# Kernel optimization log

Measured on AMD Instinct MI355X. Metric: run time of the kernel, lower is better.

The kernel has to match this reference:

```python
import jax, jax.numpy as jnp
import numpy as np

HT_H, HT_W = 512, 512          # Hough accumulator grid
SPHERE_SIZE = 32768            # Gaussian-sphere bins
NUM_VOTES = 1_500_000          # rows in vote_mapping
BATCH, CHANNEL = 2, 64         # channel % 4 == 0 required by the module


def setup_inputs() -> dict:
    key = jax.random.key(0)
    k1, k2, k3, k4 = jax.random.split(key, 4)
    x = jax.random.normal(k1, (BATCH, CHANNEL, HT_H, HT_W), dtype=jnp.float32)
    ht_idx = jax.random.randint(k2, (NUM_VOTES,), 0, HT_H * HT_W, dtype=jnp.int32)
    sphere_idx = jax.random.randint(k3, (NUM_VOTES,), 0, SPHERE_SIZE, dtype=jnp.int32)
    weight = jax.random.uniform(k4, (NUM_VOTES,), dtype=jnp.float32)
    return {"x": x, "ht_idx": ht_idx, "sphere_idx": sphere_idx, "weight": weight}


def reference(x, ht_idx, sphere_idx, weight):
    b, c, h, w = x.shape
    # SPHERE_CUDA.forward: split channels into 4 groups, flatten HT grid
    xf = x.reshape(b * 4, c // 4, h * w)              # [B4, C4, HW]
    # HT2SPHERE: gather each vote's HT cell, scale by vote weight,
    # scatter-add into its sphere bin.
    votes = xf[:, :, ht_idx] * weight                  # [B4, C4, V]
    out = jax.ops.segment_sum(
        jnp.moveaxis(votes, -1, 0), sphere_idx, num_segments=SPHERE_SIZE
    )                                                  # [S, B4, C4]
    out = jnp.moveaxis(out, 0, -1)                     # [B4, C4, S]
    return out.reshape(b, c, SPHERE_SIZE)              # [B, C, S]
```

## Files before the change

kernel.cpp:

```cpp
#include <hip/hip_runtime.h>
#include <stdint.h>


#define S_BINS   32768
#define NBUCKET  1024
#define BINS     32
#define CAP      2048
#define CHUNK    8192
#define MAXRB    192
#define HT_BITS  18

__device__ __forceinline__ unsigned bf16_rne(float f) {
    unsigned u = __float_as_uint(f);
    return (u + 0x7FFFu + ((u >> 16) & 1u)) >> 16;
}

__global__ __launch_bounds__(512) void fused_tr_kernel(
    const float* __restrict__ x, uint32_t* __restrict__ xTb, int HW,
    const int* __restrict__ ht, const int* __restrict__ sp,
    const float* __restrict__ w,
    uint2* __restrict__ records, int* __restrict__ blkcur,
    int V, int nrb) {
    __shared__ __align__(16) char smem[69696];
    const int t = threadIdx.x;
    if ((int)blockIdx.x < nrb) {
        uint2* rec  = (uint2*)smem;
        int*   hcur = (int*)(smem + 65536);
        int*   wsum = (int*)(smem + 69632);
        const int blk = blockIdx.x;
        const int lane = t & 63, wv = t >> 6;
        const int base = blk * CHUNK, end = min(V, base + CHUNK), n = end - base;
        hcur[2 * t] = 0; hcur[2 * t + 1] = 0;
        __syncthreads();
        for (int v = base + t; v < end; v += 512) atomicAdd(&hcur[sp[v] >> 5], 1);
        __syncthreads();
        const int l0 = hcur[2 * t], l1 = hcur[2 * t + 1];
        const int tot = l0 + l1;
        int sc = tot;
#pragma unroll
        for (int off = 1; off < 64; off <<= 1) {
            const int up = __shfl_up(sc, off);
            if (lane >= off) sc += up;
        }
        if (lane == 63) wsum[wv] = sc;
        __syncthreads();
        if (wv == 0 && lane < 8) {
            const int v0 = wsum[lane];
            int s = v0;
#pragma unroll
            for (int off = 1; off < 8; off <<= 1) {
                const int up = __shfl_up(s, off);
                if (lane >= off) s += up;
            }
            wsum[lane] = s - v0;
        }
        __syncthreads();
        const int run = wsum[wv] + (sc - tot);
        hcur[2 * t]     = run;
        hcur[2 * t + 1] = run + l0;
        __syncthreads();
        for (int v = base + t; v < end; v += 512) {
            const int s = sp[v];
            const int b = s >> 5, sl = s & 31;
            const int pos = atomicAdd(&hcur[b], 1);
            rec[pos] = make_uint2((unsigned)ht[v] | ((unsigned)sl << HT_BITS),
                                  __float_as_uint(w[v]));
        }
        __syncthreads();
        for (int i = t; i < n; i += 512)
            records[(size_t)blk * CHUNK + i] = rec[i];
        blkcur[(size_t)blk * NBUCKET + 2 * t]     = hcur[2 * t];
        blkcur[(size_t)blk * NBUCKET + 2 * t + 1] = hcur[2 * t + 1];
    } else {
        float* tile = (float*)smem;
        const int ht0 = ((int)blockIdx.x - nrb) * 64;
        for (int e = t; e < 128 * 16; e += 512) {
            const int ch = e >> 4, hq = e & 15;
            const float4 v = *(const float4*)(x + (size_t)ch * HW + ht0 + 4 * hq);
            const int a = 4 * hq;
            tile[(a + 0) * 129 + ch] = v.x;
            tile[(a + 1) * 129 + ch] = v.y;
            tile[(a + 2) * 129 + ch] = v.z;
            tile[(a + 3) * 129 + ch] = v.w;
        }
        __syncthreads();
        for (int e = t; e < 64 * 32; e += 512) {
            const int hl = e >> 5, cp = (e & 31) * 2;
            const unsigned lo0 = bf16_rne(tile[hl * 129 + cp]);
            const unsigned hi0 = bf16_rne(tile[hl * 129 + cp + 64]);
            const unsigned lo1 = bf16_rne(tile[hl * 129 + cp + 1]);
            const unsigned hi1 = bf16_rne(tile[hl * 129 + cp + 65]);
            *(uint2*)(xTb + (size_t)(ht0 + hl) * 64 + cp) =
                make_uint2(lo0 | (hi0 << 16), lo1 | (hi1 << 16));
        }
    }
}

__global__ __launch_bounds__(512) void accum_kernel(
    const uint32_t* __restrict__ xTb, const uint2* __restrict__ records,
    const int* __restrict__ blkcur, int nrb, float* __restrict__ out) {
    __shared__ uint2 sorted[CAP];
    __shared__ __align__(16) char rawbuf[BINS * 129 * 4];
    __shared__ int hist[BINS], off[BINS + 1], cur[BINS];
    __shared__ int segcnt[MAXRB], segpos[MAXRB];
    __shared__ int ntot;
    uint2* raw = (uint2*)rawbuf;
    const uint4* xTb4 = (const uint4*)xTb;
    const int bkt = blockIdx.x, t = threadIdx.x;
    const int lane = t & 63, wv = t >> 6;
    const int q = lane >> 4, ql = lane & 15;
    float a[4][8];
#pragma unroll
    for (int i = 0; i < 4; ++i)
#pragma unroll
        for (int j = 0; j < 8; ++j) a[i][j] = 0.f;

    if (t < BINS) hist[t] = 0;
    int s0 = 0;
    if (t < nrb) {
        const int e1 = blkcur[(size_t)t * NBUCKET + bkt];
        s0 = (bkt == 0) ? 0 : blkcur[(size_t)t * NBUCKET + bkt - 1];
        segcnt[t] = e1 - s0;
    }
    __syncthreads();
    if (wv == 0) {
        int carry = 0;
        for (int b0 = 0; b0 < nrb; b0 += 64) {
            const int idx = b0 + lane;
            const int c = (idx < nrb) ? segcnt[idx] : 0;
            int sc = c;
#pragma unroll
            for (int off2 = 1; off2 < 64; off2 <<= 1) {
                const int up = __shfl_up(sc, off2);
                if (lane >= off2) sc += up;
            }
            if (idx < nrb) segpos[idx] = carry + sc - c;
            carry += __shfl(sc, 63);
        }
        if (lane == 0) ntot = carry;
    }
    __syncthreads();
    const int n = min(ntot, CAP);
    if (t < nrb) {
        const int cnt = segcnt[t];
        const int p = segpos[t];
        const uint2* src = records + (size_t)t * CHUNK + s0;
        for (int j = 0; j < cnt; ++j) {
            const int d = p + j;
            if (d < CAP) {
                const uint2 r = src[j];
                raw[d] = r;
                atomicAdd(&hist[(r.x >> HT_BITS) & 31], 1);
            }
        }
    }
    __syncthreads();
    if (t == 0) {
        int run = 0;
        for (int j = 0; j < BINS; ++j) { off[j] = run; cur[j] = run; run += hist[j]; }
        off[BINS] = run;
    }
    __syncthreads();
    for (int i = t; i < n; i += 512) {
        const uint2 r = raw[i];
        const int pos = atomicAdd(&cur[(r.x >> HT_BITS) & 31], 1);
        sorted[pos] = r;
    }
    __syncthreads();
#pragma unroll
    for (int bb = 0; bb < 4; ++bb) {
        const int f = wv * 4 + bb;
        const int s0f = off[f], s1f = off[f + 1];
#pragma unroll 1
        for (int k = s0f; k < s1f; k += 16) {
#pragma unroll
            for (int u = 0; u < 4; ++u) {
                const int kk = k + 4 * u + q;
                if (kk < s1f) {
                    const uint2 r = sorted[kk];
                    const uint4 g = xTb4[(size_t)(r.x & 0x3FFFF) * 16 + ql];
                    const float wt = __uint_as_float(r.y);
                    a[bb][0] += __uint_as_float(g.x << 16)          * wt;
                    a[bb][1] += __uint_as_float(g.x & 0xFFFF0000u)  * wt;
                    a[bb][2] += __uint_as_float(g.y << 16)          * wt;
                    a[bb][3] += __uint_as_float(g.y & 0xFFFF0000u)  * wt;
                    a[bb][4] += __uint_as_float(g.z << 16)          * wt;
                    a[bb][5] += __uint_as_float(g.z & 0xFFFF0000u)  * wt;
                    a[bb][6] += __uint_as_float(g.w << 16)          * wt;
                    a[bb][7] += __uint_as_float(g.w & 0xFFFF0000u)  * wt;
                }
            }
        }
    }
#pragma unroll
    for (int bb = 0; bb < 4; ++bb)
#pragma unroll
        for (int j = 0; j < 8; ++j) {
            a[bb][j] += __shfl_xor(a[bb][j], 16);
            a[bb][j] += __shfl_xor(a[bb][j], 32);
        }
    __syncthreads();
    float* epi = (float*)rawbuf;
    if (lane < 16) {
#pragma unroll
        for (int bb = 0; bb < 4; ++bb) {
            const int f = wv * 4 + bb;
            epi[f * 129 + 4 * ql]      = a[bb][0];
            epi[f * 129 + 4 * ql + 64] = a[bb][1];
            epi[f * 129 + 4 * ql + 1]  = a[bb][2];
            epi[f * 129 + 4 * ql + 65] = a[bb][3];
            epi[f * 129 + 4 * ql + 2]  = a[bb][4];
            epi[f * 129 + 4 * ql + 66] = a[bb][5];
            epi[f * 129 + 4 * ql + 3]  = a[bb][6];
            epi[f * 129 + 4 * ql + 67] = a[bb][7];
        }
    }
    __syncthreads();
    for (int i = t; i < 128 * BINS; i += 512) {
        const int ch = i >> 5, bin = i & 31;
        out[(size_t)ch * S_BINS + bkt * BINS + bin] = epi[bin * 129 + ch];
    }
}

__global__ void direct_kernel(const float* __restrict__ x,
                              const int* __restrict__ ht_idx,
                              const int* __restrict__ sp_idx,
                              const float* __restrict__ weight,
                              float* __restrict__ out, int V, int HW, int S,
                              int CH) {
    const int v = blockIdx.x * 2 + (threadIdx.x >> 7);
    if (v >= V) return;
    const int ch = threadIdx.x & 127;
    if (ch >= CH) return;
    atomicAdd(&out[(size_t)ch * S + sp_idx[v]],
              x[(size_t)ch * HW + ht_idx[v]] * weight[v]);
}

extern "C" void kernel_launch(void* const* d_in, const int* in_sizes, int n_in,
                              void* d_out, int out_size, void* d_ws, size_t ws_size,
                              hipStream_t stream) {
    const float* x  = (const float*)d_in[0];
    const int*   ht = (const int*)d_in[1];
    const int*   sp = (const int*)d_in[2];
    const float* w  = (const float*)d_in[3];
    float* out = (float*)d_out;

    const int HW = 512 * 512;
    const int CH = in_sizes[0] / HW;
    const int S  = out_size / CH;
    const int V  = in_sizes[1];
    const int nrb = (V + CHUNK - 1) / CHUNK;
    const int ntb = HW / 64;

    const size_t xTb_bytes = (size_t)CH * HW * sizeof(uint16_t);
    const size_t rec_bytes = (size_t)MAXRB * CHUNK * sizeof(uint2);
    const size_t cur_bytes = (size_t)MAXRB * NBUCKET * sizeof(int);
    const size_t need = xTb_bytes + rec_bytes + cur_bytes;

    if (CH == 128 && S == S_BINS && HW == (1 << HT_BITS) && nrb <= MAXRB &&
        ws_size >= need) {
        char* p = (char*)d_ws;
        uint32_t* xTb  = (uint32_t*)p;  p += xTb_bytes;
        uint2* records = (uint2*)p;     p += rec_bytes;
        int* blkcur    = (int*)p;

        fused_tr_kernel<<<nrb + ntb, 512, 0, stream>>>(
            x, xTb, HW, ht, sp, w, records, blkcur, V, nrb);
        accum_kernel<<<NBUCKET, 512, 0, stream>>>(xTb, records, blkcur, nrb,
                                                  out);
    } else {
        hipMemsetAsync(out, 0, (size_t)out_size * sizeof(float), stream);
        direct_kernel<<<(V + 1) / 2, 256, 0, stream>>>(x, ht, sp, w, out, V, HW,
                                                       S, CH);
    }
}
```

Baseline: 303.0 us.

## Parallelize record gather via binary search and make accumulation branchless

The serial per-segment record copy, where each of up to nrb threads walks its own segment, is replaced by a flat loop over all records. Each of the 512 threads finds its source segment by binary search over the segment prefix offsets, which spreads the global loads evenly. The accumulation loop now clamps the index and zeroes the weight for out-of-range slots instead of branching, and unrolls by 2 to allow more loads in flight. Accumulators are kept per bin and written to shared memory right after each bin, which lowers register pressure at the cost of some redundant loads on tail slots.

```diff
diff --git a/kernel.cpp b/kernel.cpp
--- a/kernel.cpp
+++ b/kernel.cpp
@@ -102,25 +102,21 @@
     __shared__ uint2 sorted[CAP];
     __shared__ __align__(16) char rawbuf[BINS * 129 * 4];
     __shared__ int hist[BINS], off[BINS + 1], cur[BINS];
-    __shared__ int segcnt[MAXRB], segpos[MAXRB];
+    __shared__ int segcnt[MAXRB], segpos[MAXRB], segs0[MAXRB];
     __shared__ int ntot;
     uint2* raw = (uint2*)rawbuf;
+    float* epi = (float*)rawbuf;
     const uint4* xTb4 = (const uint4*)xTb;
     const int bkt = blockIdx.x, t = threadIdx.x;
     const int lane = t & 63, wv = t >> 6;
     const int q = lane >> 4, ql = lane & 15;
-    float a[4][8];
-#pragma unroll
-    for (int i = 0; i < 4; ++i)
-#pragma unroll
-        for (int j = 0; j < 8; ++j) a[i][j] = 0.f;
 
     if (t < BINS) hist[t] = 0;
-    int s0 = 0;
     if (t < nrb) {
         const int e1 = blkcur[(size_t)t * NBUCKET + bkt];
-        s0 = (bkt == 0) ? 0 : blkcur[(size_t)t * NBUCKET + bkt - 1];
+        const int s0 = (bkt == 0) ? 0 : blkcur[(size_t)t * NBUCKET + bkt - 1];
         segcnt[t] = e1 - s0;
+        segs0[t]  = s0;
     }
     __syncthreads();
     if (wv == 0) {
@@ -141,18 +137,16 @@
     }
     __syncthreads();
     const int n = min(ntot, CAP);
-    if (t < nrb) {
-        const int cnt = segcnt[t];
-        const int p = segpos[t];
-        const uint2* src = records + (size_t)t * CHUNK + s0;
-        for (int j = 0; j < cnt; ++j) {
-            const int d = p + j;
-            if (d < CAP) {
-                const uint2 r = src[j];
-                raw[d] = r;
-                atomicAdd(&hist[(r.x >> HT_BITS) & 31], 1);
-            }
-        }
+    for (int i = t; i < n; i += 512) {
+        int lo = 0, hi = nrb - 1;
+#pragma unroll
+        for (int it = 0; it < 8; ++it) {
+            const int mid = (lo + hi + 1) >> 1;
+            if (segpos[mid] <= i) lo = mid; else hi = mid - 1;
+        }
+        const uint2 r = records[(size_t)lo * CHUNK + segs0[lo] + (i - segpos[lo])];
+        raw[i] = r;
+        atomicAdd(&hist[(r.x >> HT_BITS) & 31], 1);
     }
     __syncthreads();
     if (t == 0) {
@@ -167,52 +161,48 @@
         sorted[pos] = r;
     }
     __syncthreads();
-#pragma unroll
+#pragma unroll 1
     for (int bb = 0; bb < 4; ++bb) {
         const int f = wv * 4 + bb;
         const int s0f = off[f], s1f = off[f + 1];
-#pragma unroll 1
+        float a0 = 0.f, a1 = 0.f, a2 = 0.f, a3 = 0.f;
+        float a4 = 0.f, a5 = 0.f, a6 = 0.f, a7 = 0.f;
+#pragma unroll 2
         for (int k = s0f; k < s1f; k += 16) {
 #pragma unroll
             for (int u = 0; u < 4; ++u) {
                 const int kk = k + 4 * u + q;
-                if (kk < s1f) {
-                    const uint2 r = sorted[kk];
-                    const uint4 g = xTb4[(size_t)(r.x & 0x3FFFF) * 16 + ql];
-                    const float wt = __uint_as_float(r.y);
-                    a[bb][0] += __uint_as_float(g.x << 16)          * wt;
-                    a[bb][1] += __uint_as_float(g.x & 0xFFFF0000u)  * wt;
-                    a[bb][2] += __uint_as_float(g.y << 16)          * wt;
-                    a[bb][3] += __uint_as_float(g.y & 0xFFFF0000u)  * wt;
-                    a[bb][4] += __uint_as_float(g.z << 16)          * wt;
-                    a[bb][5] += __uint_as_float(g.z & 0xFFFF0000u)  * wt;
-                    a[bb][6] += __uint_as_float(g.w << 16)          * wt;
-                    a[bb][7] += __uint_as_float(g.w & 0xFFFF0000u)  * wt;
-                }
+                const int kc = min(kk, s1f - 1);
+                const uint2 r = sorted[kc];
+                const uint4 g = xTb4[(size_t)(r.x & 0x3FFFF) * 16 + ql];
+                const float wt = (kk < s1f) ? __uint_as_float(r.y) : 0.f;
+                a0 += __uint_as_float(g.x << 16)          * wt;
+                a1 += __uint_as_float(g.x & 0xFFFF0000u)  * wt;
+                a2 += __uint_as_float(g.y << 16)          * wt;
+                a3 += __uint_as_float(g.y & 0xFFFF0000u)  * wt;
+                a4 += __uint_as_float(g.z << 16)          * wt;
+                a5 += __uint_as_float(g.z & 0xFFFF0000u)  * wt;
+                a6 += __uint_as_float(g.w << 16)          * wt;
+                a7 += __uint_as_float(g.w & 0xFFFF0000u)  * wt;
             }
         }
-    }
-#pragma unroll
-    for (int bb = 0; bb < 4; ++bb)
-#pragma unroll
-        for (int j = 0; j < 8; ++j) {
-            a[bb][j] += __shfl_xor(a[bb][j], 16);
-            a[bb][j] += __shfl_xor(a[bb][j], 32);
-        }
-    __syncthreads();
-    float* epi = (float*)rawbuf;
-    if (lane < 16) {
-#pragma unroll
-        for (int bb = 0; bb < 4; ++bb) {
-            const int f = wv * 4 + bb;
-            epi[f * 129 + 4 * ql]      = a[bb][0];
-            epi[f * 129 + 4 * ql + 64] = a[bb][1];
-            epi[f * 129 + 4 * ql + 1]  = a[bb][2];
-            epi[f * 129 + 4 * ql + 65] = a[bb][3];
-            epi[f * 129 + 4 * ql + 2]  = a[bb][4];
-            epi[f * 129 + 4 * ql + 66] = a[bb][5];
-            epi[f * 129 + 4 * ql + 3]  = a[bb][6];
-            epi[f * 129 + 4 * ql + 67] = a[bb][7];
+        a0 += __shfl_xor(a0, 16); a0 += __shfl_xor(a0, 32);
+        a1 += __shfl_xor(a1, 16); a1 += __shfl_xor(a1, 32);
+        a2 += __shfl_xor(a2, 16); a2 += __shfl_xor(a2, 32);
+        a3 += __shfl_xor(a3, 16); a3 += __shfl_xor(a3, 32);
+        a4 += __shfl_xor(a4, 16); a4 += __shfl_xor(a4, 32);
+        a5 += __shfl_xor(a5, 16); a5 += __shfl_xor(a5, 32);
+        a6 += __shfl_xor(a6, 16); a6 += __shfl_xor(a6, 32);
+        a7 += __shfl_xor(a7, 16); a7 += __shfl_xor(a7, 32);
+        if (lane < 16) {
+            epi[f * 129 + 4 * ql]      = a0;
+            epi[f * 129 + 4 * ql + 64] = a1;
+            epi[f * 129 + 4 * ql + 1]  = a2;
+            epi[f * 129 + 4 * ql + 65] = a3;
+            epi[f * 129 + 4 * ql + 2]  = a4;
+            epi[f * 129 + 4 * ql + 66] = a5;
+            epi[f * 129 + 4 * ql + 3]  = a6;
+            epi[f * 129 + 4 * ql + 67] = a7;
         }
     }
     __syncthreads();
```

Result: faster. 281.0 us (-7.3%).
